# Optimization experiments

Hardware: AMD Instinct MI355X
Metric: run time of the kernel (lower is better)

## Reference

```python
import jax, jax.numpy as jnp
import numpy as np

E, H, DK, DV, HID, B, S = 512, 8, 64, 64, 2048, 8, 1024
EPS = 1e-15


def _ln(x, g, b):
    m = x.mean(-1, keepdims=True)
    v = ((x - m) ** 2).mean(-1, keepdims=True)  # unbiased=False
    return g * (x - m) / jnp.sqrt(v + EPS) + b


def _mha(x, kv, Wq, bq, Wk, bk, Wv, bv, Wo, bo, causal):
    # Wq/Wk: [H, DK, E], Wv: [H, DV, E] -- stacked per-head nn.Linear weights
    q = jnp.einsum('bse,hde->bhsd', x, Wq) + bq[None, :, None, :]
    k = jnp.einsum('bte,hde->bhtd', kv, Wk) + bk[None, :, None, :]
    v = jnp.einsum('bte,hde->bhtd', kv, Wv) + bv[None, :, None, :]
    scale = jnp.sqrt(jnp.asarray(q.shape[-1], q.dtype))
    s = jnp.einsum('bhsd,bhtd->bhst', q, k) / scale
    if causal:
        Sq, Tk = s.shape[-2], s.shape[-1]
        mask = jnp.triu(jnp.full((Sq, Tk), -jnp.inf, dtype=s.dtype), k=1)
        s = s + mask[None, None]
    p = jax.nn.softmax(s, axis=-1)
    o = jnp.einsum('bhst,bhtd->bhsd', p, v)
    b_, h_, s_, d_ = o.shape
    o = o.transpose(0, 2, 1, 3).reshape(b_, s_, h_ * d_)
    return o @ Wo.T + bo


def setup_inputs() -> dict:
    key = jax.random.key(0)
    ks = iter(jax.random.split(key, 40))

    def n(shape, s=0.02):
        return jax.random.normal(next(ks), shape, dtype=jnp.float32) * s

    inp = {
        'dec_input': jax.random.normal(next(ks), (B, S, E), dtype=jnp.float32),
        'enc_output': jax.random.normal(next(ks), (B, S, E), dtype=jnp.float32),
        # masked self-attention params
        'Wq1': n((H, DK, E)), 'bq1': jnp.zeros((H, DK), jnp.float32),
        'Wk1': n((H, DK, E)), 'bk1': jnp.zeros((H, DK), jnp.float32),
        'Wv1': n((H, DV, E)), 'bv1': jnp.zeros((H, DV), jnp.float32),
        'Wo1': n((E, H * DV)), 'bo1': jnp.zeros((E,), jnp.float32),
        # cross-attention params
        'Wq2': n((H, DK, E)), 'bq2': jnp.zeros((H, DK), jnp.float32),
        'Wk2': n((H, DK, E)), 'bk2': jnp.zeros((H, DK), jnp.float32),
        'Wv2': n((H, DV, E)), 'bv2': jnp.zeros((H, DV), jnp.float32),
        'Wo2': n((E, H * DV)), 'bo2': jnp.zeros((E,), jnp.float32),
        # feedforward params
        'Wf1': n((HID, E)), 'bf1': jnp.zeros((HID,), jnp.float32),
        'Wf2': n((E, HID)), 'bf2': jnp.zeros((E,), jnp.float32),
        # layer norm params
        'g1': jnp.ones((E,), jnp.float32), 'be1': jnp.zeros((E,), jnp.float32),
        'g2': jnp.ones((E,), jnp.float32), 'be2': jnp.zeros((E,), jnp.float32),
        'g3': jnp.ones((E,), jnp.float32), 'be3': jnp.zeros((E,), jnp.float32),
    }
    return inp


def reference(dec_input, enc_output,
              Wq1, bq1, Wk1, bk1, Wv1, bv1, Wo1, bo1,
              Wq2, bq2, Wk2, bk2, Wv2, bv2, Wo2, bo2,
              Wf1, bf1, Wf2, bf2,
              g1, be1, g2, be2, g3, be3):
    # masked multi-head self-attention + residual + norm
    a = _mha(dec_input, dec_input, Wq1, bq1, Wk1, bk1, Wv1, bv1, Wo1, bo1, True)
    x = _ln(dec_input + a, g1, be1)
    # cross-attention with encoder output + residual + norm
    c = _mha(x, enc_output, Wq2, bq2, Wk2, bk2, Wv2, bv2, Wo2, bo2, False)
    x = _ln(x + c, g2, be2)
    # position-wise feedforward + residual + norm (dropout=0 -> identity)
    f = jax.nn.relu(x @ Wf1.T + bf1) @ Wf2.T + bf2
    return _ln(x + f, g3, be3)
```

## Files before the change

### kernel.cpp

```cpp
#include <hip/hip_runtime.h>
#include <cstddef>

#define EDIM   512
#define HHEADS 8
#define DHEAD  64
#define HIDDIM 2048
#define BATCH  8
#define SEQ    1024
#define MTOK   (BATCH*SEQ)

typedef __bf16 bf16;
typedef __attribute__((ext_vector_type(8))) __bf16 bf16x8;
typedef __attribute__((ext_vector_type(4))) __bf16 bf16x4;
typedef __attribute__((ext_vector_type(4))) float f32x4;

__device__ __forceinline__ void gl_lds16(const bf16* g, bf16* l) {
  __builtin_amdgcn_global_load_lds(
      (const __attribute__((address_space(1))) unsigned int*)g,
      (__attribute__((address_space(3))) unsigned int*)l, 16, 0, 0);
}

struct WPtrs { const float* p[10]; };

__global__ __launch_bounds__(256)
void convert_weights(WPtrs w, bf16* __restrict__ dst) {
  const size_t v = ((size_t)blockIdx.x * 256 + threadIdx.x) * 4;
  const float* src;
  size_t off;
  if (v < 2097152) { src = w.p[v >> 18]; off = v & 262143; }
  else { const size_t v2 = v - 2097152; src = w.p[8 + (v2 >> 20)]; off = v2 & 1048575; }
  const float4 f = *reinterpret_cast<const float4*>(src + off);
  bf16x4 o;
  o[0] = (bf16)f.x; o[1] = (bf16)f.y; o[2] = (bf16)f.z; o[3] = (bf16)f.w;
  *reinterpret_cast<bf16x4*>(dst + v) = o;
}

__global__ __launch_bounds__(256)
void f2b_kernel(const float* __restrict__ src, bf16* __restrict__ dst) {
  const size_t i = (size_t)blockIdx.x * 256 + threadIdx.x;
  const float4 f = reinterpret_cast<const float4*>(src)[i];
  bf16x4 o;
  o[0] = (bf16)f.x; o[1] = (bf16)f.y; o[2] = (bf16)f.z; o[3] = (bf16)f.w;
  reinterpret_cast<bf16x4*>(dst)[i] = o;
}

__device__ __forceinline__ void stage_tile(const bf16* Ag, const bf16* Wg, int Kdim,
                                           int k0, bf16* AsBuf, bf16* WsBuf,
                                           int w, int srow, int scol) {
  #pragma unroll
  for (int c = 0; c < 4; ++c)
    gl_lds16(Ag + (size_t)((w + c*4)*8 + srow) * Kdim + k0 + scol, &AsBuf[(w + c*4) * 512]);
  #pragma unroll
  for (int c = 0; c < 2; ++c)
    gl_lds16(Wg + (size_t)((w + c*4)*8 + srow) * Kdim + k0 + scol, &WsBuf[(w + c*4) * 512]);
}

template<int OM, bool RELU>
__global__ __launch_bounds__(256)
void gemm_bf16(const bf16* __restrict__ A, const bf16* __restrict__ W,
               const float* __restrict__ bias, const float* __restrict__ bias2,
               const float* __restrict__ bias3,
               void* __restrict__ C0, void* __restrict__ C1, void* __restrict__ C2,
               float scale, int seg_base, int Ndim, int Kdim, int NXB) {
  constexpr int MI = 2, NI = 4;

  __shared__ bf16 As[2][128 * 64];
  __shared__ bf16 Ws[2][64 * 64];
  const int tid  = threadIdx.x;
  const int lane = tid & 63;
  const int w    = tid >> 6;
  const int lin  = blockIdx.x;
  const int xcd  = lin & 7;
  const int loc  = lin >> 3;
  const int nx   = loc % NXB;
  const int myl  = loc / NXB;
  const int bm   = (xcd * 8 + myl) * 128;
  const int bn   = nx * 64;
  const int frow = lane & 15;
  const int lg   = lane >> 4;
  const int srow = lane >> 3;
  const int scol = ((lane & 7) ^ srow) * 8;
  const bf16* Ag = A + (size_t)bm * Kdim;
  const bf16* Wg = W + (size_t)bn * Kdim;

  f32x4 acc[MI][NI] = {};

  const int nsteps = Kdim / 64;

  stage_tile(Ag, Wg, Kdim, 0,  As[0], Ws[0], w, srow, scol);
  __builtin_amdgcn_sched_barrier(0);
  stage_tile(Ag, Wg, Kdim, 64, As[1], Ws[1], w, srow, scol);
  __builtin_amdgcn_sched_barrier(0);

  for (int s = 0; s < nsteps; ++s) {
    const int cur = s & 1;
    if (s + 1 < nsteps) asm volatile("s_waitcnt vmcnt(6)" ::: "memory");
    else                asm volatile("s_waitcnt vmcnt(0)" ::: "memory");
    __builtin_amdgcn_s_barrier();
    __builtin_amdgcn_sched_barrier(0);

    bf16x8 af[MI][2], wf[NI][2];
    #pragma unroll
    for (int mi = 0; mi < MI; ++mi)
      #pragma unroll
      for (int kk = 0; kk < 2; ++kk) {
        const int row  = w*32 + mi*16 + frow;
        const int phys = (kk*4 + lg) ^ (frow & 7);
        af[mi][kk] = *reinterpret_cast<const bf16x8*>(&As[cur][row*64 + phys*8]);
      }
    #pragma unroll
    for (int ni = 0; ni < NI; ++ni)
      #pragma unroll
      for (int kk = 0; kk < 2; ++kk) {
        const int row  = ni*16 + frow;
        const int phys = (kk*4 + lg) ^ (frow & 7);
        wf[ni][kk] = *reinterpret_cast<const bf16x8*>(&Ws[cur][row*64 + phys*8]);
      }
    #pragma unroll
    for (int kk = 0; kk < 2; ++kk)
      #pragma unroll
      for (int mi = 0; mi < MI; ++mi)
        #pragma unroll
        for (int ni = 0; ni < NI; ++ni)
          acc[mi][ni] = __builtin_amdgcn_mfma_f32_16x16x32_bf16(
              af[mi][kk], wf[ni][kk], acc[mi][ni], 0, 0, 0);

    __builtin_amdgcn_sched_barrier(0);
    __builtin_amdgcn_s_barrier();
    __builtin_amdgcn_sched_barrier(0);
    if (s + 2 < nsteps)
      stage_tile(Ag, Wg, Kdim, (s + 2) * 64, As[cur], Ws[cur], w, srow, scol);
  }

  const int ccol = lane & 15;
  const int crow = (lane >> 4) * 4;
  #pragma unroll
  for (int mi = 0; mi < MI; ++mi) {
    #pragma unroll
    for (int ni = 0; ni < NI; ++ni) {
      const int col  = bn + ni*16 + ccol;
      const int row0 = bm + w*32 + mi*16 + crow;
      if (OM == 0) {
        float* C = (float*)C0;
        const float bv = bias[col];
        #pragma unroll
        for (int j = 0; j < 4; ++j) {
          float vv = acc[mi][ni][j] + bv;
          if (RELU) vv = fmaxf(vv, 0.0f);
          C[(size_t)(row0 + j) * Ndim + col] = vv;
        }
      } else if (OM == 1) {
        bf16* C = (bf16*)C0;
        const float bv = bias[col];
        #pragma unroll
        for (int j = 0; j < 4; ++j) {
          float vv = acc[mi][ni][j] + bv;
          if (RELU) vv = fmaxf(vv, 0.0f);
          C[(size_t)(row0 + j) * Ndim + col] = (bf16)(vv * scale);
        }
      } else {
        const int seg = (col >> 9) + seg_base;
        const int cl  = col & 511;
        if (seg == 0) {
          bf16* C = (bf16*)C0;
          const float bv = bias[cl];
          #pragma unroll
          for (int j = 0; j < 4; ++j)
            C[(size_t)(row0 + j) * EDIM + cl] = (bf16)((acc[mi][ni][j] + bv) * scale);
        } else if (seg == 1) {
          bf16* C = (bf16*)C1;
          const float bv = bias2[cl];
          #pragma unroll
          for (int j = 0; j < 4; ++j)
            C[(size_t)(row0 + j) * EDIM + cl] = (bf16)(acc[mi][ni][j] + bv);
        } else {
          bf16* C = (bf16*)C2;
          const float bv = bias3[cl];
          bf16x4 pk;
          #pragma unroll
          for (int j = 0; j < 4; ++j) pk[j] = (bf16)(acc[mi][ni][j] + bv);
          const int bb = row0 >> 10, s0 = row0 & 1023;
          const int hh = cl >> 6,   dd = cl & 63;
          *reinterpret_cast<bf16x4*>(
              &C[((size_t)((bb * HHEADS + hh) * DHEAD + dd)) * SEQ + s0]) = pk;
        }
      }
    }
  }
}

#define APITCH 72

template<bool CAUSAL>
__global__ __launch_bounds__(256)
void attn_mfma(const bf16* __restrict__ Q, const bf16* __restrict__ K,
               const bf16* __restrict__ Vt, bf16* __restrict__ O) {
  __shared__ bf16 Ks[64][APITCH];
  __shared__ bf16 Vs[64][APITCH];
  __shared__ bf16 Pl[4][16][APITCH];

  const int lin = blockIdx.x;
  const int h   = lin & 7;
  const int loc = lin >> 3;
  const int qt  = loc & 15;
  const int b   = loc >> 4;
  const int tid  = threadIdx.x;
  const int lane = tid & 63;
  const int w    = tid >> 6;
  const int l15  = lane & 15;
  const int lg   = lane >> 4;

  const size_t qrow = (size_t)(b * SEQ + qt * 64 + w * 16 + l15);
  const bf16x8 qf0 = *reinterpret_cast<const bf16x8*>(&Q[qrow * EDIM + h * DHEAD + lg * 8]);
  const bf16x8 qf1 = *reinterpret_cast<const bf16x8*>(&Q[qrow * EDIM + h * DHEAD + 32 + lg * 8]);

  float m_i[4], l_i[4];
  f32x4 oacc[4] = {};
  #pragma unroll
  for (int r = 0; r < 4; ++r) { m_i[r] = -1e30f; l_i[r] = 0.0f; }

  const int r0 = tid >> 3;
  const int c0 = (tid & 7) * 8;
  const size_t kbase = (size_t)(b * SEQ) * EDIM + h * DHEAD;
  const size_t vbase = ((size_t)(b * HHEADS + h) * DHEAD) * SEQ;

  const int njt = CAUSAL ? (qt + 1) : (SEQ / 64);

  bf16x8 pk0, pk1, pv0, pv1;
  pk0 = *reinterpret_cast<const bf16x8*>(&K[kbase + (size_t)r0 * EDIM + c0]);
  pk1 = *reinterpret_cast<const bf16x8*>(&K[kbase + (size_t)(r0 + 32) * EDIM + c0]);
  pv0 = *reinterpret_cast<const bf16x8*>(&Vt[vbase + (size_t)r0 * SEQ + c0]);
  pv1 = *reinterpret_cast<const bf16x8*>(&Vt[vbase + (size_t)(r0 + 32) * SEQ + c0]);

  for (int jt = 0; jt < njt; ++jt) {
    __syncthreads();
    *reinterpret_cast<bf16x8*>(&Ks[r0][c0])      = pk0;
    *reinterpret_cast<bf16x8*>(&Ks[r0 + 32][c0]) = pk1;
    *reinterpret_cast<bf16x8*>(&Vs[r0][c0])      = pv0;
    *reinterpret_cast<bf16x8*>(&Vs[r0 + 32][c0]) = pv1;
    __syncthreads();

    if (jt + 1 < njt) {
      const size_t ko = kbase + (size_t)((jt + 1) * 64) * EDIM;
      pk0 = *reinterpret_cast<const bf16x8*>(&K[ko + (size_t)r0 * EDIM + c0]);
      pk1 = *reinterpret_cast<const bf16x8*>(&K[ko + (size_t)(r0 + 32) * EDIM + c0]);
      const size_t vo = vbase + (size_t)(jt + 1) * 64;
      pv0 = *reinterpret_cast<const bf16x8*>(&Vt[vo + (size_t)r0 * SEQ + c0]);
      pv1 = *reinterpret_cast<const bf16x8*>(&Vt[vo + (size_t)(r0 + 32) * SEQ + c0]);
    }

    f32x4 sf[4] = {};
    #pragma unroll
    for (int ni = 0; ni < 4; ++ni) {
      const bf16x8 kf0 = *reinterpret_cast<const bf16x8*>(&Ks[l15 + 16*ni][lg * 8]);
      const bf16x8 kf1 = *reinterpret_cast<const bf16x8*>(&Ks[l15 + 16*ni][32 + lg * 8]);
      sf[ni] = __builtin_amdgcn_mfma_f32_16x16x32_bf16(qf0, kf0, sf[ni], 0, 0, 0);
      sf[ni] = __builtin_amdgcn_mfma_f32_16x16x32_bf16(qf1, kf1, sf[ni], 0, 0, 0);
    }

    if (CAUSAL && jt == qt) {
      #pragma unroll
      for (int ni = 0; ni < 4; ++ni)
        #pragma unroll
        for (int r = 0; r < 4; ++r)
          if (l15 + 16*ni > w*16 + lg*4 + r) sf[ni][r] = -1e30f;
    }

    #pragma unroll
    for (int r = 0; r < 4; ++r) {
      float rm = fmaxf(fmaxf(sf[0][r], sf[1][r]), fmaxf(sf[2][r], sf[3][r]));
      rm = fmaxf(rm, __shfl_xor(rm, 1, 16));
      rm = fmaxf(rm, __shfl_xor(rm, 2, 16));
      rm = fmaxf(rm, __shfl_xor(rm, 4, 16));
      rm = fmaxf(rm, __shfl_xor(rm, 8, 16));
      const float mn   = fmaxf(m_i[r], rm);
      const float corr = __expf(m_i[r] - mn);
      float p[4], rs = 0.0f;
      #pragma unroll
      for (int ni = 0; ni < 4; ++ni) { p[ni] = __expf(sf[ni][r] - mn); rs += p[ni]; }
      rs += __shfl_xor(rs, 1, 16); rs += __shfl_xor(rs, 2, 16);
      rs += __shfl_xor(rs, 4, 16); rs += __shfl_xor(rs, 8, 16);
      l_i[r] = l_i[r] * corr + rs;
      m_i[r] = mn;
      #pragma unroll
      for (int ni = 0; ni < 4; ++ni) {
        oacc[ni][r] *= corr;
        Pl[w][lg*4 + r][l15 + 16*ni] = (bf16)p[ni];
      }
    }

    #pragma unroll
    for (int ks = 0; ks < 2; ++ks) {
      const bf16x8 pf = *reinterpret_cast<const bf16x8*>(&Pl[w][l15][ks*32 + lg*8]);
      #pragma unroll
      for (int ni = 0; ni < 4; ++ni) {
        const bf16x8 vf = *reinterpret_cast<const bf16x8*>(&Vs[l15 + 16*ni][ks*32 + lg*8]);
        oacc[ni] = __builtin_amdgcn_mfma_f32_16x16x32_bf16(pf, vf, oacc[ni], 0, 0, 0);
      }
    }
  }

  #pragma unroll
  for (int r = 0; r < 4; ++r) {
    const float inv = 1.0f / l_i[r];
    const size_t orow = (size_t)(b * SEQ + qt * 64 + w * 16 + lg * 4 + r);
    #pragma unroll
    for (int ni = 0; ni < 4; ++ni)
      O[orow * EDIM + h * DHEAD + l15 + 16*ni] = (bf16)(oacc[ni][r] * inv);
  }
}

template<bool EMITB>
__global__ __launch_bounds__(256)
void add_ln_kernel(const float* __restrict__ X, const float* __restrict__ Ain,
                   const float* __restrict__ g, const float* __restrict__ bb,
                   float* __restrict__ out, bf16* __restrict__ outb) {
  const int row = blockIdx.x;
  const int tid = threadIdx.x;
  __shared__ float red[4];
  const size_t base = (size_t)row * EDIM;

  const float v0 = X[base + tid]       + Ain[base + tid];
  const float v1 = X[base + tid + 256] + Ain[base + tid + 256];

  float s = v0 + v1;
  #pragma unroll
  for (int off = 32; off; off >>= 1) s += __shfl_down(s, off);
  if ((tid & 63) == 0) red[tid >> 6] = s;
  __syncthreads();
  const float mean = (red[0] + red[1] + red[2] + red[3]) * (1.0f / EDIM);
  __syncthreads();

  const float d0 = v0 - mean, d1 = v1 - mean;
  float vs = d0 * d0 + d1 * d1;
  #pragma unroll
  for (int off = 32; off; off >>= 1) vs += __shfl_down(vs, off);
  if ((tid & 63) == 0) red[tid >> 6] = vs;
  __syncthreads();
  const float var = (red[0] + red[1] + red[2] + red[3]) * (1.0f / EDIM);
  const float rstd = rsqrtf(var + 1e-15f);

  const float r0v = g[tid]       * (d0 * rstd) + bb[tid];
  const float r1v = g[tid + 256] * (d1 * rstd) + bb[tid + 256];
  out[base + tid]       = r0v;
  out[base + tid + 256] = r1v;
  if (EMITB) {
    outb[base + tid]       = (bf16)r0v;
    outb[base + tid + 256] = (bf16)r1v;
  }
}

extern "C" void kernel_launch(void* const* d_in, const int* in_sizes, int n_in,
                              void* d_out, int out_size, void* d_ws, size_t ws_size,
                              hipStream_t stream) {
  const float* dec = (const float*)d_in[0];
  const float* enc = (const float*)d_in[1];
  const float* Wq1 = (const float*)d_in[2];  const float* bq1 = (const float*)d_in[3];
  const float* Wk1 = (const float*)d_in[4];  const float* bk1 = (const float*)d_in[5];
  const float* Wv1 = (const float*)d_in[6];  const float* bv1 = (const float*)d_in[7];
  const float* Wo1 = (const float*)d_in[8];  const float* bo1 = (const float*)d_in[9];
  const float* Wq2 = (const float*)d_in[10]; const float* bq2 = (const float*)d_in[11];
  const float* Wk2 = (const float*)d_in[12]; const float* bk2 = (const float*)d_in[13];
  const float* Wv2 = (const float*)d_in[14]; const float* bv2 = (const float*)d_in[15];
  const float* Wo2 = (const float*)d_in[16]; const float* bo2 = (const float*)d_in[17];
  const float* Wf1 = (const float*)d_in[18]; const float* bf1 = (const float*)d_in[19];
  const float* Wf2 = (const float*)d_in[20]; const float* bf2 = (const float*)d_in[21];
  const float* g1  = (const float*)d_in[22]; const float* be1 = (const float*)d_in[23];
  const float* g2  = (const float*)d_in[24]; const float* be2 = (const float*)d_in[25];
  const float* g3  = (const float*)d_in[26]; const float* be3 = (const float*)d_in[27];
  float* out = (float*)d_out;

  char*  wsb  = (char*)d_ws;
  bf16*  decb = (bf16*)(wsb);
  bf16*  encb = (bf16*)(wsb + ((size_t)8  << 20));
  bf16*  qb   = (bf16*)(wsb + ((size_t)16 << 20));
  bf16*  kb   = (bf16*)(wsb + ((size_t)24 << 20));
  bf16*  vtb  = (bf16*)(wsb + ((size_t)32 << 20));
  bf16*  aob  = (bf16*)(wsb + ((size_t)40 << 20));
  float* x1   = (float*)(wsb + ((size_t)48 << 20));
  float* x2   = (float*)(wsb + ((size_t)64 << 20));
  float* t0   = (float*)(wsb + ((size_t)80 << 20));
  bf16*  wbf  = (bf16*)(wsb + ((size_t)96 << 20));
  bf16*  x1b  = decb;
  bf16*  x2b  = aob;
  bf16*  hidb = (bf16*)(wsb);

  bf16* wq1 = wbf + 0;
  bf16* wo1 = wbf + 786432;
  bf16* wq2 = wbf + 1048576;
  bf16* wk2 = wbf + 1310720;
  bf16* wo2 = wbf + 1835008;
  bf16* wf1 = wbf + 2097152;  bf16* wf2 = wbf + 3145728;

  const dim3 blk(256);
  const dim3 gP64(8 * 64);
  const dim3 gQKV(24 * 64);
  const dim3 gKV(16 * 64);
  const dim3 gF1(32 * 64);
  const dim3 gAttn(1024);

  WPtrs wp;
  wp.p[0] = Wq1; wp.p[1] = Wk1; wp.p[2] = Wv1; wp.p[3] = Wo1;
  wp.p[4] = Wq2; wp.p[5] = Wk2; wp.p[6] = Wv2; wp.p[7] = Wo2;
  wp.p[8] = Wf1; wp.p[9] = Wf2;
  convert_weights<<<dim3(4096), blk, 0, stream>>>(wp, wbf);
  f2b_kernel<<<dim3(4096), blk, 0, stream>>>(dec, decb);
  f2b_kernel<<<dim3(4096), blk, 0, stream>>>(enc, encb);

  gemm_bf16<3, false><<<gQKV, blk, 0, stream>>>(
      decb, wq1, bq1, bk1, bv1, qb, kb, vtb, 0.125f, 0, 1536, EDIM, 24);
  attn_mfma<true><<<gAttn, blk, 0, stream>>>(qb, kb, vtb, aob);
  gemm_bf16<0, false><<<gP64, blk, 0, stream>>>(
      aob, wo1, bo1, nullptr, nullptr, t0, nullptr, nullptr, 1.0f, 0, EDIM, EDIM, 8);
  add_ln_kernel<true><<<dim3(MTOK), blk, 0, stream>>>(dec, t0, g1, be1, x1, x1b);

  gemm_bf16<1, false><<<gP64, blk, 0, stream>>>(
      x1b, wq2, bq2, nullptr, nullptr, qb, nullptr, nullptr, 0.125f, 0, EDIM, EDIM, 8);
  gemm_bf16<3, false><<<gKV, blk, 0, stream>>>(
      encb, wk2, nullptr, bk2, bv2, nullptr, kb, vtb, 1.0f, 1, 1024, EDIM, 16);
  attn_mfma<false><<<gAttn, blk, 0, stream>>>(qb, kb, vtb, aob);
  gemm_bf16<0, false><<<gP64, blk, 0, stream>>>(
      aob, wo2, bo2, nullptr, nullptr, t0, nullptr, nullptr, 1.0f, 0, EDIM, EDIM, 8);
  add_ln_kernel<true><<<dim3(MTOK), blk, 0, stream>>>(x1, t0, g2, be2, x2, x2b);

  gemm_bf16<1, true><<<gF1, blk, 0, stream>>>(
      x2b, wf1, bf1, nullptr, nullptr, hidb, nullptr, nullptr, 1.0f, 0, HIDDIM, EDIM, 32);
  gemm_bf16<0, false><<<gP64, blk, 0, stream>>>(
      hidb, wf2, bf2, nullptr, nullptr, t0, nullptr, nullptr, 1.0f, 0, EDIM, HIDDIM, 8);
  add_ln_kernel<false><<<dim3(MTOK), blk, 0, stream>>>(x2, t0, g3, be3, out, nullptr);

  (void)in_sizes; (void)n_in; (void)out_size; (void)ws_size;
}
```

Baseline: 437.5 us.

## Enlarge GEMM tile to 128x128 with 2x2 wave layout; raise MFMA priority in attention

The bf16 GEMM now computes a 128x128 output tile per block instead of 128x64. Waves are arranged 2x2, each owning a 64x64 sub-tile with 4x4 MFMA accumulators, and fragments are loaded per k-slice. This raises arithmetic intensity and halves the grid sizes, which aims to cut global/LDS traffic per flop, at the cost of more registers, more LDS and fewer blocks. Separately, the attention kernel wraps its MFMA sections in s_setprio so matrix work gets scheduling priority over other waves.

```diff
diff --git a/kernel.cpp b/kernel.cpp
--- a/kernel.cpp
+++ b/kernel.cpp
@@ -49,10 +49,10 @@
                                            int w, int srow, int scol) {
   #pragma unroll
   for (int c = 0; c < 4; ++c)
-    gl_lds16(Ag + (size_t)((w + c*4)*8 + srow) * Kdim + k0 + scol, &AsBuf[(w + c*4) * 512]);
-  #pragma unroll
-  for (int c = 0; c < 2; ++c)
-    gl_lds16(Wg + (size_t)((w + c*4)*8 + srow) * Kdim + k0 + scol, &WsBuf[(w + c*4) * 512]);
+    gl_lds16(Ag + (size_t)((w*4 + c)*8 + srow) * Kdim + k0 + scol, &AsBuf[(w*4 + c) * 512]);
+  #pragma unroll
+  for (int c = 0; c < 4; ++c)
+    gl_lds16(Wg + (size_t)((w*4 + c)*8 + srow) * Kdim + k0 + scol, &WsBuf[(w*4 + c) * 512]);
 }
 
 template<int OM, bool RELU>
@@ -62,20 +62,21 @@
                const float* __restrict__ bias3,
                void* __restrict__ C0, void* __restrict__ C1, void* __restrict__ C2,
                float scale, int seg_base, int Ndim, int Kdim, int NXB) {
-  constexpr int MI = 2, NI = 4;
+  constexpr int MI = 4, NI = 4;
 
   __shared__ bf16 As[2][128 * 64];
-  __shared__ bf16 Ws[2][64 * 64];
+  __shared__ bf16 Ws[2][128 * 64];
   const int tid  = threadIdx.x;
   const int lane = tid & 63;
   const int w    = tid >> 6;
+  const int wr   = w >> 1, wc = w & 1;
   const int lin  = blockIdx.x;
   const int xcd  = lin & 7;
   const int loc  = lin >> 3;
   const int nx   = loc % NXB;
   const int myl  = loc / NXB;
   const int bm   = (xcd * 8 + myl) * 128;
-  const int bn   = nx * 64;
+  const int bn   = nx * 128;
   const int frow = lane & 15;
   const int lg   = lane >> 4;
   const int srow = lane >> 3;
@@ -94,36 +95,33 @@
 
   for (int s = 0; s < nsteps; ++s) {
     const int cur = s & 1;
-    if (s + 1 < nsteps) asm volatile("s_waitcnt vmcnt(6)" ::: "memory");
+    if (s + 1 < nsteps) asm volatile("s_waitcnt vmcnt(8)" ::: "memory");
     else                asm volatile("s_waitcnt vmcnt(0)" ::: "memory");
     __builtin_amdgcn_s_barrier();
     __builtin_amdgcn_sched_barrier(0);
 
-    bf16x8 af[MI][2], wf[NI][2];
-    #pragma unroll
-    for (int mi = 0; mi < MI; ++mi)
-      #pragma unroll
-      for (int kk = 0; kk < 2; ++kk) {
-        const int row  = w*32 + mi*16 + frow;
+    #pragma unroll
+    for (int kk = 0; kk < 2; ++kk) {
+      bf16x8 af[MI], wf[NI];
+      #pragma unroll
+      for (int mi = 0; mi < MI; ++mi) {
+        const int row  = wr*64 + mi*16 + frow;
         const int phys = (kk*4 + lg) ^ (frow & 7);
-        af[mi][kk] = *reinterpret_cast<const bf16x8*>(&As[cur][row*64 + phys*8]);
+        af[mi] = *reinterpret_cast<const bf16x8*>(&As[cur][row*64 + phys*8]);
       }
-    #pragma unroll
-    for (int ni = 0; ni < NI; ++ni)
-      #pragma unroll
-      for (int kk = 0; kk < 2; ++kk) {
-        const int row  = ni*16 + frow;
+      #pragma unroll
+      for (int ni = 0; ni < NI; ++ni) {
+        const int row  = wc*64 + ni*16 + frow;
         const int phys = (kk*4 + lg) ^ (frow & 7);
-        wf[ni][kk] = *reinterpret_cast<const bf16x8*>(&Ws[cur][row*64 + phys*8]);
+        wf[ni] = *reinterpret_cast<const bf16x8*>(&Ws[cur][row*64 + phys*8]);
       }
-    #pragma unroll
-    for (int kk = 0; kk < 2; ++kk)
       #pragma unroll
       for (int mi = 0; mi < MI; ++mi)
         #pragma unroll
         for (int ni = 0; ni < NI; ++ni)
           acc[mi][ni] = __builtin_amdgcn_mfma_f32_16x16x32_bf16(
-              af[mi][kk], wf[ni][kk], acc[mi][ni], 0, 0, 0);
+              af[mi], wf[ni], acc[mi][ni], 0, 0, 0);
+    }
 
     __builtin_amdgcn_sched_barrier(0);
     __builtin_amdgcn_s_barrier();
@@ -138,8 +136,8 @@
   for (int mi = 0; mi < MI; ++mi) {
     #pragma unroll
     for (int ni = 0; ni < NI; ++ni) {
-      const int col  = bn + ni*16 + ccol;
-      const int row0 = bm + w*32 + mi*16 + crow;
+      const int col  = bn + wc*64 + ni*16 + ccol;
+      const int row0 = bm + wr*64 + mi*16 + crow;
       if (OM == 0) {
         float* C = (float*)C0;
         const float bv = bias[col];
@@ -250,6 +248,7 @@
     }
 
     f32x4 sf[4] = {};
+    __builtin_amdgcn_s_setprio(1);
     #pragma unroll
     for (int ni = 0; ni < 4; ++ni) {
       const bf16x8 kf0 = *reinterpret_cast<const bf16x8*>(&Ks[l15 + 16*ni][lg * 8]);
@@ -257,6 +256,7 @@
       sf[ni] = __builtin_amdgcn_mfma_f32_16x16x32_bf16(qf0, kf0, sf[ni], 0, 0, 0);
       sf[ni] = __builtin_amdgcn_mfma_f32_16x16x32_bf16(qf1, kf1, sf[ni], 0, 0, 0);
     }
+    __builtin_amdgcn_s_setprio(0);
 
     if (CAUSAL && jt == qt) {
       #pragma unroll
@@ -289,6 +289,7 @@
       }
     }
 
+    __builtin_amdgcn_s_setprio(1);
     #pragma unroll
     for (int ks = 0; ks < 2; ++ks) {
       const bf16x8 pf = *reinterpret_cast<const bf16x8*>(&Pl[w][l15][ks*32 + lg*8]);
@@ -298,6 +299,7 @@
         oacc[ni] = __builtin_amdgcn_mfma_f32_16x16x32_bf16(pf, vf, oacc[ni], 0, 0, 0);
       }
     }
+    __builtin_amdgcn_s_setprio(0);
   }
 
   #pragma unroll
@@ -393,10 +395,10 @@
   bf16* wf1 = wbf + 2097152;  bf16* wf2 = wbf + 3145728;
 
   const dim3 blk(256);
-  const dim3 gP64(8 * 64);
-  const dim3 gQKV(24 * 64);
-  const dim3 gKV(16 * 64);
-  const dim3 gF1(32 * 64);
+  const dim3 gP64(64 * 4);
+  const dim3 gQKV(64 * 12);
+  const dim3 gKV(64 * 8);
+  const dim3 gF1(64 * 16);
   const dim3 gAttn(1024);
 
   WPtrs wp;
@@ -408,25 +410,25 @@
   f2b_kernel<<<dim3(4096), blk, 0, stream>>>(enc, encb);
 
   gemm_bf16<3, false><<<gQKV, blk, 0, stream>>>(
-      decb, wq1, bq1, bk1, bv1, qb, kb, vtb, 0.125f, 0, 1536, EDIM, 24);
+      decb, wq1, bq1, bk1, bv1, qb, kb, vtb, 0.125f, 0, 1536, EDIM, 12);
   attn_mfma<true><<<gAttn, blk, 0, stream>>>(qb, kb, vtb, aob);
   gemm_bf16<0, false><<<gP64, blk, 0, stream>>>(
-      aob, wo1, bo1, nullptr, nullptr, t0, nullptr, nullptr, 1.0f, 0, EDIM, EDIM, 8);
+      aob, wo1, bo1, nullptr, nullptr, t0, nullptr, nullptr, 1.0f, 0, EDIM, EDIM, 4);
   add_ln_kernel<true><<<dim3(MTOK), blk, 0, stream>>>(dec, t0, g1, be1, x1, x1b);
 
   gemm_bf16<1, false><<<gP64, blk, 0, stream>>>(
-      x1b, wq2, bq2, nullptr, nullptr, qb, nullptr, nullptr, 0.125f, 0, EDIM, EDIM, 8);
+      x1b, wq2, bq2, nullptr, nullptr, qb, nullptr, nullptr, 0.125f, 0, EDIM, EDIM, 4);
   gemm_bf16<3, false><<<gKV, blk, 0, stream>>>(
-      encb, wk2, nullptr, bk2, bv2, nullptr, kb, vtb, 1.0f, 1, 1024, EDIM, 16);
+      encb, wk2, nullptr, bk2, bv2, nullptr, kb, vtb, 1.0f, 1, 1024, EDIM, 8);
   attn_mfma<false><<<gAttn, blk, 0, stream>>>(qb, kb, vtb, aob);
   gemm_bf16<0, false><<<gP64, blk, 0, stream>>>(
-      aob, wo2, bo2, nullptr, nullptr, t0, nullptr, nullptr, 1.0f, 0, EDIM, EDIM, 8);
+      aob, wo2, bo2, nullptr, nullptr, t0, nullptr, nullptr, 1.0f, 0, EDIM, EDIM, 4);
   add_ln_kernel<true><<<dim3(MTOK), blk, 0, stream>>>(x1, t0, g2, be2, x2, x2b);
 
   gemm_bf16<1, true><<<gF1, blk, 0, stream>>>(
-      x2b, wf1, bf1, nullptr, nullptr, hidb, nullptr, nullptr, 1.0f, 0, HIDDIM, EDIM, 32);
+      x2b, wf1, bf1, nullptr, nullptr, hidb, nullptr, nullptr, 1.0f, 0, HIDDIM, EDIM, 16);
   gemm_bf16<0, false><<<gP64, blk, 0, stream>>>(
-      hidb, wf2, bf2, nullptr, nullptr, t0, nullptr, nullptr, 1.0f, 0, EDIM, HIDDIM, 8);
+      hidb, wf2, bf2, nullptr, nullptr, t0, nullptr, nullptr, 1.0f, 0, EDIM, HIDDIM, 4);
   add_ln_kernel<false><<<dim3(MTOK), blk, 0, stream>>>(x2, t0, g3, be3, out, nullptr);
 
   (void)in_sizes; (void)n_in; (void)out_size; (void)ws_size;
```

New measurement: 418.7 us. 1.04x faster.
